# Optimization experiments

Measured on AMD Instinct MI355X. Metric: run time of the kernel, lower is better.

The kernel has to match this reference:

```python
import jax, jax.numpy as jnp
import numpy as np

B, T, W, E, H, EMB, NVOCAB, WIN = 256, 200, 200, 768, 256, 32, 201, 8


def setup_inputs() -> dict:
    key = jax.random.key(0)
    ks = jax.random.split(key, 12)
    s = 0.05
    inputs = jax.random.normal(ks[0], (B, T, E), jnp.float32)
    full_word_embeddings = jax.random.normal(ks[1], (B, W, E), jnp.float32)
    lengths = jax.random.randint(ks[2], (B,), T // 2, T + 1)
    fix = jax.random.randint(ks[3], (B, T), 1, NVOCAB)
    fix_seq = jnp.where(jnp.arange(T)[None, :] < lengths[:, None], fix, 0)
    emb_table = (jax.random.normal(ks[4], (NVOCAB, EMB)) * s).at[0].set(0.0)  # padding_idx=0
    W_ih = jax.random.normal(ks[5], (3 * H, E + EMB)) * s  # torch GRU layout, gates r,z,n
    W_hh = jax.random.normal(ks[6], (3 * H, H)) * s
    b_ih = jax.random.normal(ks[7], (3 * H,)) * s
    b_hh = jax.random.normal(ks[8], (3 * H,)) * s
    W_out = jax.random.normal(ks[9], (E, H)) * s  # output_layer: Linear(H, E)
    b_out = jnp.zeros((E,), jnp.float32)
    W_dur = jax.random.normal(ks[10], (1, H)) * s  # duration_layer: Linear(H, 1)
    b_dur = jnp.zeros((1,), jnp.float32)
    return {"inputs": inputs, "fix_seq": fix_seq, "full_word_embeddings": full_word_embeddings,
            "lengths": lengths, "expert_id": 0, "emb_table": emb_table,
            "W_ih": W_ih, "b_ih": b_ih, "W_hh": W_hh, "b_hh": b_hh,
            "W_out": W_out, "b_out": b_out, "W_dur": W_dur, "b_dur": b_dur}


def _gru(x, W_ih, b_ih, W_hh, b_hh, h_dim):
    # x: [B,T,I]. Precompute input projections once, scan over time.
    xg = jnp.einsum('bti,gi->btg', x, W_ih) + b_ih  # [B,T,3H]

    def step(h, xg_t):
        hg = h @ W_hh.T + b_hh
        xr, xz, xn = jnp.split(xg_t, 3, axis=-1)
        hr, hz, hn = jnp.split(hg, 3, axis=-1)
        r = jax.nn.sigmoid(xr + hr)
        z = jax.nn.sigmoid(xz + hz)
        n = jnp.tanh(xn + r * hn)
        h_new = (1.0 - z) * n + z * h
        return h_new, h_new

    h0 = jnp.zeros((x.shape[0], h_dim), x.dtype)
    _, outs = jax.lax.scan(step, h0, jnp.swapaxes(xg, 0, 1))
    return jnp.swapaxes(outs, 0, 1)  # [B,T,H]


def reference(inputs, fix_seq, full_word_embeddings, lengths, expert_id,
              emb_table, W_ih, b_ih, W_hh, b_hh, W_out, b_out, W_dur, b_dur):
    del expert_id  # weights of the selected expert are passed directly
    valid_mask = fix_seq != 0
    scan_emb = emb_table[fix_seq]  # [B,T,32]
    rnn_in = jnp.concatenate([inputs, scan_emb], axis=-1)
    outputs = _gru(rnn_in, W_ih, b_ih, W_hh, b_hh, W_hh.shape[1])  # [B,T,H]
    # pad_packed_sequence zeros outputs beyond each sequence length
    tmask = jnp.arange(outputs.shape[1])[None, :] < lengths[:, None]
    outputs = outputs * tmask[..., None].astype(outputs.dtype)
    # dot attention: proj then scores against word embeddings
    proj = outputs @ W_out.T + b_out  # [B,T,E]
    logits = jnp.einsum('bte,bwe->btw', proj, full_word_embeddings)
    # saccade window mask around current fixation position
    wpos = jnp.arange(full_word_embeddings.shape[1])[None, None, :]
    dist = jnp.abs(wpos - fix_seq[..., None])
    sacc = (dist <= WIN) & valid_mask[..., None]
    logits = jnp.where(sacc, logits, -1e9)
    word_mask = jnp.sum(jnp.abs(full_word_embeddings), axis=-1) != 0
    logits = jnp.where(word_mask[:, None, :], logits, -1e9)
    dur_pred = (outputs @ W_dur.T + b_dur)[..., 0]  # [B,T]
    return logits, dur_pred
```

## Files before the change

kernel.cpp:

```cpp
#include <hip/hip_runtime.h>
#include <hip/hip_bf16.h>

typedef __attribute__((ext_vector_type(8))) short bf16x8;
typedef __attribute__((ext_vector_type(4))) float f32x4;
typedef __attribute__((ext_vector_type(4))) int   i32x4;

#define NB 256
#define NT 200
#define NW 200
#define NE 768
#define NH 256
#define NEMB 32
#define KIN 800
#define G3H 768
#define MROWS 51200

__device__ __forceinline__ float bf2f(unsigned short h) {
    return __uint_as_float(((unsigned)h) << 16);
}
__device__ __forceinline__ unsigned short f2bf(float f) {
    unsigned u = __float_as_uint(f);
    u += 0x7fff + ((u >> 16) & 1);
    return (unsigned short)(u >> 16);
}
__device__ __forceinline__ float sigm(float x) { return 1.0f / (1.0f + __expf(-x)); }
__device__ __forceinline__ float tanh_fast(float x) {
    float e = __expf(2.0f * x);
    return 1.0f - 2.0f / (e + 1.0f);
}

#if __has_builtin(__builtin_amdgcn_sdot4)
__device__ __forceinline__ int SDOT4(int a, int b, int c) {
    return __builtin_amdgcn_sdot4(a, b, c, false);
}
#else
__device__ __forceinline__ int SDOT4(int a, int b, int c) {
    #pragma unroll
    for (int j = 0; j < 4; j++)
        c += (int)(signed char)(a >> (8 * j)) * (int)(signed char)(b >> (8 * j));
    return c;
}
#endif

__device__ __forceinline__ void gload16(const void* g, void* l) {
    __builtin_amdgcn_global_load_lds((const __attribute__((address_space(1))) unsigned int*)g,
                                     (__attribute__((address_space(3))) unsigned int*)l,
                                     16, 0, 0);
}

__global__ void prep1(const float* __restrict__ inputs, const int* __restrict__ fix_seq,
                      const float* __restrict__ emb, const float* __restrict__ Wih,
                      const float* __restrict__ Wout, const float* __restrict__ bih,
                      const float* __restrict__ bhh,
                      unsigned short* __restrict__ Abf, unsigned short* __restrict__ Wihbf,
                      unsigned short* __restrict__ WoutTbf, float* __restrict__ biasC,
                      float* __restrict__ bias0) {
    const long gid0 = (long)blockIdx.x * blockDim.x + threadIdx.x;
    if (gid0 < G3H) biasC[gid0] = bih[gid0] + (gid0 < 512 ? bhh[gid0] : 0.0f);
    if (gid0 < NH) bias0[gid0] = 0.0f;
    const long NA = (long)MROWS * 100;
    const long NWU = 768L * 100;
    const long NOU = 256L * 96;
    const long total = NA + NWU + NOU;
    for (long u = gid0; u < total; u += (long)gridDim.x * blockDim.x) {
        bf16x8 v;
        unsigned short* dst;
        if (u < NA) {
            long row = u / 100;
            int c8 = (int)(u % 100) * 8;
            const float* s;
            if (c8 < NE) {
                s = inputs + row * NE + c8;
            } else {
                int fx = fix_seq[row];
                s = emb + (long)fx * NEMB + (c8 - NE);
            }
            #pragma unroll
            for (int j = 0; j < 8; j++) v[j] = (short)f2bf(s[j]);
            dst = Abf + row * KIN + c8;
        } else if (u < NA + NWU) {
            long u2 = u - NA;
            long row = u2 / 100;
            int c8 = (int)(u2 % 100) * 8;
            const float* s = Wih + row * KIN + c8;
            #pragma unroll
            for (int j = 0; j < 8; j++) v[j] = (short)f2bf(s[j]);
            dst = Wihbf + row * KIN + c8;
        } else {
            long u3 = u - NA - NWU;
            long row = u3 / 96;
            int c8 = (int)(u3 % 96) * 8;
            #pragma unroll
            for (int j = 0; j < 8; j++)
                v[j] = (short)f2bf(Wout[(long)(c8 + j) * NH + row]);
            dst = WoutTbf + row * NE + c8;
        }
        *(bf16x8*)dst = v;
    }
}

__global__ __launch_bounds__(256)
void gemm_bt128(const unsigned short* __restrict__ A,
                const unsigned short* __restrict__ Bw,
                const float* __restrict__ bias,
                unsigned short* __restrict__ Out,
                int M, int N, int K) {
    __shared__ unsigned short As[128 * 32];
    __shared__ unsigned short Bs[128 * 32];
    const int bid = (int)((blockIdx.x & 7) * (gridDim.x >> 3) + (blockIdx.x >> 3));
    const int nblk = N >> 7;
    const int m0 = (bid / nblk) << 7;
    const int n0 = (bid % nblk) << 7;
    const int tid = threadIdx.x;
    const int lane = tid & 63;
    const int wave = tid >> 6;
    const int wm = (wave >> 1) << 6;
    const int wn = (wave & 1) << 6;
    const int nk = K >> 5;

    const int srow = tid >> 2;
    const int sseg = (tid & 3) << 4;
    const char* gA0 = (const char*)(A + (long)(m0 + srow) * K) + sseg;
    const char* gA1 = (const char*)(A + (long)(m0 + 64 + srow) * K) + sseg;
    const char* gB0 = (const char*)(Bw + (long)(n0 + srow) * K) + sseg;
    const char* gB1 = (const char*)(Bw + (long)(n0 + 64 + srow) * K) + sseg;
    char* lA0 = (char*)As + wave * 1024;
    char* lA1 = (char*)As + 4096 + wave * 1024;
    char* lB0 = (char*)Bs + wave * 1024;
    char* lB1 = (char*)Bs + 4096 + wave * 1024;

    f32x4 acc[4][4] = {};

    for (int kt = 0; kt < nk; kt++) {
        __syncthreads();
        gload16(gA0 + kt * 64, lA0);
        gload16(gA1 + kt * 64, lA1);
        gload16(gB0 + kt * 64, lB0);
        gload16(gB1 + kt * 64, lB1);
        asm volatile("s_waitcnt vmcnt(0)" ::: "memory");
        __syncthreads();
        bf16x8 af[4], bfr[4];
        #pragma unroll
        for (int mi = 0; mi < 4; mi++)
            af[mi] = *(const bf16x8*)((const char*)As +
                        (wm + mi * 16 + (lane & 15)) * 64 + ((lane >> 4) << 4));
        #pragma unroll
        for (int ni = 0; ni < 4; ni++)
            bfr[ni] = *(const bf16x8*)((const char*)Bs +
                        (wn + ni * 16 + (lane & 15)) * 64 + ((lane >> 4) << 4));
        #pragma unroll
        for (int mi = 0; mi < 4; mi++)
            #pragma unroll
            for (int ni = 0; ni < 4; ni++)
                acc[mi][ni] = __builtin_amdgcn_mfma_f32_16x16x32_bf16(
                                  af[mi], bfr[ni], acc[mi][ni], 0, 0, 0);
    }
    #pragma unroll
    for (int ni = 0; ni < 4; ni++) {
        const int col = n0 + wn + ni * 16 + (lane & 15);
        const float bv = bias[col];
        #pragma unroll
        for (int mi = 0; mi < 4; mi++) {
            const int row = m0 + wm + mi * 16 + ((lane >> 4) << 2);
            #pragma unroll
            for (int r = 0; r < 4; r++)
                Out[(long)(row + r) * N + col] = f2bf(acc[mi][ni][r] + bv);
        }
    }
}

__global__ __launch_bounds__(512, 2)
__attribute__((amdgpu_waves_per_eu(2, 2)))
void gru_scan(const unsigned short* __restrict__ xg,
              const float* __restrict__ Whh,
              const float* __restrict__ bhh,
              const int* __restrict__ lengths,
              unsigned short* __restrict__ hout) {
    __shared__ __align__(16) unsigned char h8[2][256];
    const int tid = threadIdx.x;
    const int lane = tid & 63;
    const int wave = tid >> 6;
    const int b = blockIdx.x;
    const int col = wave * 32 + (lane & 31);
    const int kh = lane >> 5;

    int W[3][32];
    #pragma unroll
    for (int g = 0; g < 3; g++) {
        const float* wr = Whh + (long)(g * 256 + col) * NH + kh * 128;
        #pragma unroll
        for (int d = 0; d < 32; d++) {
            const float4 f = *(const float4*)(wr + d * 4);
            unsigned pack = 0;
            #pragma unroll
            for (int j = 0; j < 4; j++) {
                const float fv = j == 0 ? f.x : j == 1 ? f.y : j == 2 ? f.z : f.w;
                int wq = (int)rintf(fv * 400.0f);
                wq = wq > 127 ? 127 : (wq < -127 ? -127 : wq);
                pack |= ((unsigned)(wq & 0xff)) << (8 * j);
            }
            W[g][d] = (int)pack;
        }
    }
    const float bhn = bhh[512 + col];
    const int len = lengths[b];
    if (tid < 128) ((unsigned*)h8)[tid] = 0u;

    const unsigned short* xrow = xg + (long)b * NT * G3H;
    unsigned short xv0 = xrow[col], xv1 = xrow[256 + col], xv2 = xrow[512 + col];
    float hp = 0.0f;
    const float ISC = 1.0f / (400.0f * 127.0f);
    const bool wlo = (lane < 32);

    asm volatile("s_waitcnt lgkmcnt(0)" ::: "memory");
    __builtin_amdgcn_sched_barrier(0);
    __builtin_amdgcn_s_barrier();
    __builtin_amdgcn_sched_barrier(0);

    for (int t = 0; t < NT; t++) {
        const unsigned char* hb = h8[(t + 1) & 1] + kh * 128;
        int p0a = 0, p0b = 0, p1a = 0, p1b = 0, p2a = 0, p2b = 0;
        #pragma unroll
        for (int r = 0; r < 8; r++) {
            const i32x4 hv = *(const i32x4*)(hb + r * 16);
            p0a = SDOT4(hv[0], W[0][r * 4 + 0], p0a);
            p1a = SDOT4(hv[0], W[1][r * 4 + 0], p1a);
            p2a = SDOT4(hv[0], W[2][r * 4 + 0], p2a);
            p0b = SDOT4(hv[1], W[0][r * 4 + 1], p0b);
            p1b = SDOT4(hv[1], W[1][r * 4 + 1], p1b);
            p2b = SDOT4(hv[1], W[2][r * 4 + 1], p2b);
            p0a = SDOT4(hv[2], W[0][r * 4 + 2], p0a);
            p1a = SDOT4(hv[2], W[1][r * 4 + 2], p1a);
            p2a = SDOT4(hv[2], W[2][r * 4 + 2], p2a);
            p0b = SDOT4(hv[3], W[0][r * 4 + 3], p0b);
            p1b = SDOT4(hv[3], W[1][r * 4 + 3], p1b);
            p2b = SDOT4(hv[3], W[2][r * 4 + 3], p2b);
        }
        int p0 = p0a + p0b, p1 = p1a + p1b, p2 = p2a + p2b;
        p0 += __shfl_xor(p0, 32);
        p1 += __shfl_xor(p1, 32);
        p2 += __shfl_xor(p2, 32);
        const float r = sigm(bf2f(xv0) + (float)p0 * ISC);
        const float z = sigm(bf2f(xv1) + (float)p1 * ISC);
        const float n = tanh_fast(bf2f(xv2) + r * ((float)p2 * ISC + bhn));
        hp = (1.0f - z) * n + z * hp;
        if (wlo) {
            h8[t & 1][col] = (unsigned char)((int)rintf(hp * 127.0f) & 0xff);
            hout[((long)b * NT + t) * NH + col] = (t < len) ? f2bf(hp) : (unsigned short)0;
        }
        if (t + 1 < NT) {
            const unsigned short* xn = xrow + (long)(t + 1) * G3H;
            xv0 = xn[col]; xv1 = xn[256 + col]; xv2 = xn[512 + col];
        }
        asm volatile("s_waitcnt lgkmcnt(0)" ::: "memory");
        __builtin_amdgcn_sched_barrier(0);
        __builtin_amdgcn_s_barrier();
        __builtin_amdgcn_sched_barrier(0);
    }
}

__global__ void prep2(const float* __restrict__ fwe, const float* __restrict__ bout,
                      unsigned short* __restrict__ fwebf,
                      unsigned char* __restrict__ wmask, float* __restrict__ dvec) {
    const int row = (int)((blockIdx.x * blockDim.x + threadIdx.x) >> 6);
    const int lane = threadIdx.x & 63;
    if (row >= MROWS) return;
    const float* s = fwe + (long)row * NE;
    unsigned short* d = fwebf + (long)row * NE;
    float asum = 0.0f, vdot = 0.0f;
    #pragma unroll
    for (int i = 0; i < 12; i++) {
        const float v = s[lane + i * 64];
        asum += fabsf(v);
        vdot += v * bout[lane + i * 64];
        d[lane + i * 64] = f2bf(v);
    }
    #pragma unroll
    for (int off = 32; off >= 1; off >>= 1) {
        asum += __shfl_xor(asum, off);
        vdot += __shfl_xor(vdot, off);
    }
    if (lane == 0) {
        wmask[row] = (asum != 0.0f) ? 1 : 0;
        dvec[row] = vdot;
    }
}

__global__ __launch_bounds__(256)
void logits_gemm(const unsigned short* __restrict__ Hrow,
                 const unsigned short* __restrict__ G,
                 const int* __restrict__ fix_seq,
                 const unsigned char* __restrict__ wmask,
                 const float* __restrict__ dvec,
                 float* __restrict__ out) {
    __shared__ unsigned short As[64 * 32];
    __shared__ unsigned short Bs[64 * 32];
    const int blk = blockIdx.x;
    const int b = blk >> 4;
    const int mt = (blk >> 2) & 3;
    const int ntile = blk & 3;
    const int t0 = mt << 6;
    const int w0 = ntile << 6;
    const int tid = threadIdx.x;
    const int lane = tid & 63;
    const int wave = tid >> 6;
    const int wm = (wave >> 1) << 5;
    const int wn = (wave & 1) << 5;

    const int srow = tid >> 2;
    const int sseg = (tid & 3) << 4;
    const int tA = t0 + srow > 199 ? 199 : t0 + srow;
    const int wB = w0 + srow > 199 ? 199 : w0 + srow;
    const char* ga = (const char*)(Hrow + ((long)b * NT + tA) * NH) + sseg;
    const char* gb = (const char*)(G + ((long)b * NW + wB) * NH) + sseg;
    char* la = (char*)As + wave * 1024;
    char* lb = (char*)Bs + wave * 1024;

    f32x4 acc[2][2] = {};
    for (int kt = 0; kt < 8; kt++) {
        __syncthreads();
        gload16(ga + kt * 64, la);
        gload16(gb + kt * 64, lb);
        asm volatile("s_waitcnt vmcnt(0)" ::: "memory");
        __syncthreads();
        bf16x8 af[2], bfr[2];
        #pragma unroll
        for (int mi = 0; mi < 2; mi++)
            af[mi] = *(const bf16x8*)((const char*)As +
                        (wm + mi * 16 + (lane & 15)) * 64 + ((lane >> 4) << 4));
        #pragma unroll
        for (int ni = 0; ni < 2; ni++)
            bfr[ni] = *(const bf16x8*)((const char*)Bs +
                        (wn + ni * 16 + (lane & 15)) * 64 + ((lane >> 4) << 4));
        #pragma unroll
        for (int mi = 0; mi < 2; mi++)
            #pragma unroll
            for (int ni = 0; ni < 2; ni++)
                acc[mi][ni] = __builtin_amdgcn_mfma_f32_16x16x32_bf16(
                                  af[mi], bfr[ni], acc[mi][ni], 0, 0, 0);
    }
    #pragma unroll
    for (int mi = 0; mi < 2; mi++) {
        #pragma unroll
        for (int r = 0; r < 4; r++) {
            const int t = t0 + wm + mi * 16 + ((lane >> 4) << 2) + r;
            if (t >= NT) continue;
            const int fx = fix_seq[b * NT + t];
            #pragma unroll
            for (int ni = 0; ni < 2; ni++) {
                const int w = w0 + wn + ni * 16 + (lane & 15);
                if (w >= NW) continue;
                int d = w - fx; d = d < 0 ? -d : d;
                const bool ok = (fx != 0) && (d <= 8) && (wmask[b * NW + w] != 0);
                out[(long)b * (NT * NW) + t * NW + w] =
                    ok ? acc[mi][ni][r] + dvec[b * NW + w] : -1e9f;
            }
        }
    }
}

__global__ void dur_kernel(const unsigned short* __restrict__ hout,
                           const float* __restrict__ Wdur, const float* __restrict__ bdur,
                           float* __restrict__ out) {
    const int row = (int)((blockIdx.x * blockDim.x + threadIdx.x) >> 6);
    const int lane = threadIdx.x & 63;
    if (row >= MROWS) return;
    const unsigned short* hp = hout + (long)row * NH + lane * 4;
    const uint2 hv = *(const uint2*)hp;
    const float4 wv = *(const float4*)(Wdur + lane * 4);
    float s = bf2f((unsigned short)(hv.x & 0xffff)) * wv.x
            + bf2f((unsigned short)(hv.x >> 16)) * wv.y
            + bf2f((unsigned short)(hv.y & 0xffff)) * wv.z
            + bf2f((unsigned short)(hv.y >> 16)) * wv.w;
    #pragma unroll
    for (int off = 32; off >= 1; off >>= 1) s += __shfl_down(s, off);
    if (lane == 0) out[(long)NB * NT * NW + row] = s + bdur[0];
}

extern "C" void kernel_launch(void* const* d_in, const int* in_sizes, int n_in,
                              void* d_out, int out_size, void* d_ws, size_t ws_size,
                              hipStream_t stream) {
    (void)in_sizes; (void)n_in; (void)out_size; (void)ws_size;
    const float* inputs  = (const float*)d_in[0];
    const int*   fix_seq = (const int*)d_in[1];
    const float* fwe     = (const float*)d_in[2];
    const int*   lengths = (const int*)d_in[3];
    const float* emb     = (const float*)d_in[5];
    const float* Wih     = (const float*)d_in[6];
    const float* bih     = (const float*)d_in[7];
    const float* Whh     = (const float*)d_in[8];
    const float* bhh     = (const float*)d_in[9];
    const float* Wout    = (const float*)d_in[10];
    const float* bout    = (const float*)d_in[11];
    const float* Wdur    = (const float*)d_in[12];
    const float* bdur    = (const float*)d_in[13];
    float* out = (float*)d_out;

    char* ws = (char*)d_ws;
    unsigned short* Abf     = (unsigned short*)(ws);
    unsigned short* xgbf    = (unsigned short*)(ws + 81920000);
    unsigned short* hout    = (unsigned short*)(ws + 160563200);
    unsigned short* Wihbf   = (unsigned short*)(ws + 186777600);
    unsigned short* WoutTbf = (unsigned short*)(ws + 188006400);
    unsigned char*  wmask   = (unsigned char*)(ws + 188399616);
    float*          biasC   = (float*)(ws + 188450816);
    float*          dvec    = (float*)(ws + 188453888);
    float*          bias0   = (float*)(ws + 188658688);
    unsigned short* fwebf   = Abf;
    unsigned short* Gbf     = xgbf;

    prep1<<<2048, 256, 0, stream>>>(inputs, fix_seq, emb, Wih, Wout, bih, bhh,
                                    Abf, Wihbf, WoutTbf, biasC, bias0);
    gemm_bt128<<<400 * 6, 256, 0, stream>>>(Abf, Wihbf, biasC, xgbf, MROWS, G3H, KIN);
    prep2<<<12800, 256, 0, stream>>>(fwe, bout, fwebf, wmask, dvec);
    gru_scan<<<256, 512, 0, stream>>>(xgbf, Whh, bhh, lengths, hout);
    gemm_bt128<<<400 * 2, 256, 0, stream>>>(fwebf, WoutTbf, bias0, Gbf, MROWS, NH, NE);
    logits_gemm<<<4096, 256, 0, stream>>>(hout, Gbf, fix_seq, wmask, dvec, out);
    dur_kernel<<<12800, 256, 0, stream>>>(hout, Wdur, bdur, out);
}
```

Before: 522.1 us.

## Compute only saccade-window logits with duration fused in, and double-buffer the GEMM

The dense per-batch logits GEMM is replaced by a per-row wave kernel. It computes dot products only for the 17 words inside the saccade window around each fixation and writes -1e9 everywhere else, and it also computes the duration output, so the separate duration kernel is removed. The main bf16 GEMM also gets ping-pong LDS buffers, so the next K tile's loads are issued while MFMAs run on the current tile. Skipping the masked entries removes most of the logits MMA work and the extra launch. The cost is scalar FMA dot products instead of MFMA, double the GEMM LDS footprint, and reliance on the barrier to cover outstanding async loads.

New measurement: 508.6 us. -2.6%, faster.

```diff
diff --git a/kernel.cpp b/kernel.cpp
--- a/kernel.cpp
+++ b/kernel.cpp
@@ -105,8 +105,8 @@
                 const float* __restrict__ bias,
                 unsigned short* __restrict__ Out,
                 int M, int N, int K) {
-    __shared__ unsigned short As[128 * 32];
-    __shared__ unsigned short Bs[128 * 32];
+    __shared__ unsigned short As[2][128 * 32];
+    __shared__ unsigned short Bs[2][128 * 32];
     const int bid = (int)((blockIdx.x & 7) * (gridDim.x >> 3) + (blockIdx.x >> 3));
     const int nblk = N >> 7;
     const int m0 = (bid / nblk) << 7;
@@ -124,29 +124,32 @@
     const char* gA1 = (const char*)(A + (long)(m0 + 64 + srow) * K) + sseg;
     const char* gB0 = (const char*)(Bw + (long)(n0 + srow) * K) + sseg;
     const char* gB1 = (const char*)(Bw + (long)(n0 + 64 + srow) * K) + sseg;
-    char* lA0 = (char*)As + wave * 1024;
-    char* lA1 = (char*)As + 4096 + wave * 1024;
-    char* lB0 = (char*)Bs + wave * 1024;
-    char* lB1 = (char*)Bs + 4096 + wave * 1024;
+    const int lofs = wave * 1024;
 
     f32x4 acc[4][4] = {};
 
+    gload16(gA0, (char*)As[0] + lofs);
+    gload16(gA1, (char*)As[0] + 4096 + lofs);
+    gload16(gB0, (char*)Bs[0] + lofs);
+    gload16(gB1, (char*)Bs[0] + 4096 + lofs);
+    __syncthreads();
+
+    int cur = 0;
     for (int kt = 0; kt < nk; kt++) {
-        __syncthreads();
-        gload16(gA0 + kt * 64, lA0);
-        gload16(gA1 + kt * 64, lA1);
-        gload16(gB0 + kt * 64, lB0);
-        gload16(gB1 + kt * 64, lB1);
-        asm volatile("s_waitcnt vmcnt(0)" ::: "memory");
-        __syncthreads();
+        if (kt + 1 < nk) {
+            gload16(gA0 + (kt + 1) * 64, (char*)As[cur ^ 1] + lofs);
+            gload16(gA1 + (kt + 1) * 64, (char*)As[cur ^ 1] + 4096 + lofs);
+            gload16(gB0 + (kt + 1) * 64, (char*)Bs[cur ^ 1] + lofs);
+            gload16(gB1 + (kt + 1) * 64, (char*)Bs[cur ^ 1] + 4096 + lofs);
+        }
         bf16x8 af[4], bfr[4];
         #pragma unroll
         for (int mi = 0; mi < 4; mi++)
-            af[mi] = *(const bf16x8*)((const char*)As +
+            af[mi] = *(const bf16x8*)((const char*)As[cur] +
                         (wm + mi * 16 + (lane & 15)) * 64 + ((lane >> 4) << 4));
         #pragma unroll
         for (int ni = 0; ni < 4; ni++)
-            bfr[ni] = *(const bf16x8*)((const char*)Bs +
+            bfr[ni] = *(const bf16x8*)((const char*)Bs[cur] +
                         (wn + ni * 16 + (lane & 15)) * 64 + ((lane >> 4) << 4));
         #pragma unroll
         for (int mi = 0; mi < 4; mi++)
@@ -154,6 +157,8 @@
             for (int ni = 0; ni < 4; ni++)
                 acc[mi][ni] = __builtin_amdgcn_mfma_f32_16x16x32_bf16(
                                   af[mi], bfr[ni], acc[mi][ni], 0, 0, 0);
+        __syncthreads();
+        cur ^= 1;
     }
     #pragma unroll
     for (int ni = 0; ni < 4; ni++) {
@@ -287,94 +292,74 @@
 }
 
 __global__ __launch_bounds__(256)
-void logits_gemm(const unsigned short* __restrict__ Hrow,
-                 const unsigned short* __restrict__ G,
-                 const int* __restrict__ fix_seq,
-                 const unsigned char* __restrict__ wmask,
-                 const float* __restrict__ dvec,
-                 float* __restrict__ out) {
-    __shared__ unsigned short As[64 * 32];
-    __shared__ unsigned short Bs[64 * 32];
-    const int blk = blockIdx.x;
-    const int b = blk >> 4;
-    const int mt = (blk >> 2) & 3;
-    const int ntile = blk & 3;
-    const int t0 = mt << 6;
-    const int w0 = ntile << 6;
-    const int tid = threadIdx.x;
-    const int lane = tid & 63;
-    const int wave = tid >> 6;
-    const int wm = (wave >> 1) << 5;
-    const int wn = (wave & 1) << 5;
-
-    const int srow = tid >> 2;
-    const int sseg = (tid & 3) << 4;
-    const int tA = t0 + srow > 199 ? 199 : t0 + srow;
-    const int wB = w0 + srow > 199 ? 199 : w0 + srow;
-    const char* ga = (const char*)(Hrow + ((long)b * NT + tA) * NH) + sseg;
-    const char* gb = (const char*)(G + ((long)b * NW + wB) * NH) + sseg;
-    char* la = (char*)As + wave * 1024;
-    char* lb = (char*)Bs + wave * 1024;
-
-    f32x4 acc[2][2] = {};
-    for (int kt = 0; kt < 8; kt++) {
-        __syncthreads();
-        gload16(ga + kt * 64, la);
-        gload16(gb + kt * 64, lb);
-        asm volatile("s_waitcnt vmcnt(0)" ::: "memory");
-        __syncthreads();
-        bf16x8 af[2], bfr[2];
-        #pragma unroll
-        for (int mi = 0; mi < 2; mi++)
-            af[mi] = *(const bf16x8*)((const char*)As +
-                        (wm + mi * 16 + (lane & 15)) * 64 + ((lane >> 4) << 4));
-        #pragma unroll
-        for (int ni = 0; ni < 2; ni++)
-            bfr[ni] = *(const bf16x8*)((const char*)Bs +
-                        (wn + ni * 16 + (lane & 15)) * 64 + ((lane >> 4) << 4));
-        #pragma unroll
-        for (int mi = 0; mi < 2; mi++)
-            #pragma unroll
-            for (int ni = 0; ni < 2; ni++)
-                acc[mi][ni] = __builtin_amdgcn_mfma_f32_16x16x32_bf16(
-                                  af[mi], bfr[ni], acc[mi][ni], 0, 0, 0);
-    }
-    #pragma unroll
-    for (int mi = 0; mi < 2; mi++) {
-        #pragma unroll
-        for (int r = 0; r < 4; r++) {
-            const int t = t0 + wm + mi * 16 + ((lane >> 4) << 2) + r;
-            if (t >= NT) continue;
-            const int fx = fix_seq[b * NT + t];
-            #pragma unroll
-            for (int ni = 0; ni < 2; ni++) {
-                const int w = w0 + wn + ni * 16 + (lane & 15);
-                if (w >= NW) continue;
-                int d = w - fx; d = d < 0 ? -d : d;
-                const bool ok = (fx != 0) && (d <= 8) && (wmask[b * NW + w] != 0);
-                out[(long)b * (NT * NW) + t * NW + w] =
-                    ok ? acc[mi][ni][r] + dvec[b * NW + w] : -1e9f;
+void logits_dur(const unsigned short* __restrict__ Hrow,
+                const unsigned short* __restrict__ G,
+                const int* __restrict__ fix_seq,
+                const unsigned char* __restrict__ wmask,
+                const float* __restrict__ dvec,
+                const float* __restrict__ Wdur, const float* __restrict__ bdur,
+                float* __restrict__ out) {
+    __shared__ float dots[4][20];
+    const int wv = threadIdx.x >> 6;
+    const int gwave = (int)blockIdx.x * 4 + wv;
+    const int lane = threadIdx.x & 63;
+    const int l16 = lane & 15;
+    const int grp = lane >> 4;
+    const int b = gwave / NT;
+
+    const unsigned short* hp = Hrow + (long)gwave * NH + l16 * 16;
+    const bf16x8 h0 = *(const bf16x8*)hp;
+    const bf16x8 h1 = *(const bf16x8*)(hp + 8);
+    float hf[16];
+    #pragma unroll
+    for (int j = 0; j < 8; j++) { hf[j] = bf2f((unsigned short)h0[j]);
+                                  hf[8 + j] = bf2f((unsigned short)h1[j]); }
+
+    const int fix = fix_seq[gwave];
+    const int wbase = fix - 8;
+
+    if (fix != 0) {
+        #pragma unroll
+        for (int it = 0; it < 5; it++) {
+            const int wi = it * 4 + grp;
+            int w = wbase + wi;
+            w = w < 0 ? 0 : (w > NW - 1 ? NW - 1 : w);
+            const unsigned short* gp = G + ((long)b * NW + w) * NH + l16 * 16;
+            const bf16x8 g0 = *(const bf16x8*)gp;
+            const bf16x8 g1 = *(const bf16x8*)(gp + 8);
+            float p = 0.0f;
+            #pragma unroll
+            for (int j = 0; j < 8; j++) {
+                p += hf[j] * bf2f((unsigned short)g0[j]);
+                p += hf[8 + j] * bf2f((unsigned short)g1[j]);
             }
-        }
-    }
-}
-
-__global__ void dur_kernel(const unsigned short* __restrict__ hout,
-                           const float* __restrict__ Wdur, const float* __restrict__ bdur,
-                           float* __restrict__ out) {
-    const int row = (int)((blockIdx.x * blockDim.x + threadIdx.x) >> 6);
-    const int lane = threadIdx.x & 63;
-    if (row >= MROWS) return;
-    const unsigned short* hp = hout + (long)row * NH + lane * 4;
-    const uint2 hv = *(const uint2*)hp;
-    const float4 wv = *(const float4*)(Wdur + lane * 4);
-    float s = bf2f((unsigned short)(hv.x & 0xffff)) * wv.x
-            + bf2f((unsigned short)(hv.x >> 16)) * wv.y
-            + bf2f((unsigned short)(hv.y & 0xffff)) * wv.z
-            + bf2f((unsigned short)(hv.y >> 16)) * wv.w;
-    #pragma unroll
-    for (int off = 32; off >= 1; off >>= 1) s += __shfl_down(s, off);
-    if (lane == 0) out[(long)NB * NT * NW + row] = s + bdur[0];
+            p += __shfl_xor(p, 1); p += __shfl_xor(p, 2);
+            p += __shfl_xor(p, 4); p += __shfl_xor(p, 8);
+            if (l16 == 0 && wi < 17) dots[wv][wi] = p;
+        }
+    }
+    float pd = 0.0f;
+    #pragma unroll
+    for (int j = 0; j < 16; j++) pd += hf[j] * Wdur[l16 * 16 + j];
+    pd += __shfl_xor(pd, 1); pd += __shfl_xor(pd, 2);
+    pd += __shfl_xor(pd, 4); pd += __shfl_xor(pd, 8);
+    if (lane == 0) out[(long)NB * NT * NW + gwave] = pd + bdur[0];
+
+    __syncthreads();
+
+    if (lane < 50) {
+        float4 o;
+        #pragma unroll
+        for (int c = 0; c < 4; c++) {
+            const int w = lane * 4 + c;
+            const int wi = w - wbase;
+            const int wic = wi < 0 ? 0 : (wi > 16 ? 16 : wi);
+            const bool ok = (fix != 0) && ((unsigned)wi < 17u) && (wmask[b * NW + w] != 0);
+            const float val = dots[wv][wic] + dvec[b * NW + w];
+            ((float*)&o)[c] = ok ? val : -1e9f;
+        }
+        *(float4*)(out + (long)gwave * NW + lane * 4) = o;
+    }
 }
 
 extern "C" void kernel_launch(void* const* d_in, const int* in_sizes, int n_in,
@@ -415,6 +400,5 @@
     prep2<<<12800, 256, 0, stream>>>(fwe, bout, fwebf, wmask, dvec);
     gru_scan<<<256, 512, 0, stream>>>(xgbf, Whh, bhh, lengths, hout);
     gemm_bt128<<<400 * 2, 256, 0, stream>>>(fwebf, WoutTbf, bias0, Gbf, MROWS, NH, NE);
-    logits_gemm<<<4096, 256, 0, stream>>>(hout, Gbf, fix_seq, wmask, dvec, out);
-    dur_kernel<<<12800, 256, 0, stream>>>(hout, Wdur, bdur, out);
-}
+    logits_dur<<<12800, 256, 0, stream>>>(hout, Gbf, fix_seq, wmask, dvec, Wdur, bdur, out);
+}
```
